# Kernel tuning notes

Measured on AMD Instinct MI355X. Metric: run time of the kernel, lower is better.

The kernel has to match this reference:

```python
import jax, jax.numpy as jnp
import numpy as np

N = 100000   # nodes
E = 800000   # edges
IN, H, OUT = 128, 128, 100  # in_channels, hidden_channels, out_channels


def _layernorm(x, g, b, eps=1e-5):
    m = jnp.mean(x, axis=-1, keepdims=True)
    v = jnp.var(x, axis=-1, keepdims=True)
    return (x - m) * jax.lax.rsqrt(v + eps) * g + b


def _sage_mean(x, src, dst, wl, bl, wr, n):
    # PyG SAGEConv(aggr='mean'): lin_l(mean_j x_j) + lin_r(x)
    s = jax.ops.segment_sum(x[src], dst, num_segments=n)               # [n, d]
    cnt = jax.ops.segment_sum(jnp.ones_like(dst, jnp.float32), dst, num_segments=n)
    aggr = s / jnp.maximum(cnt, 1.0)[:, None]
    return aggr @ wl + bl + x @ wr


def _sage_max(x, src, dst, wl, bl, wr, n):
    # PyG SAGEConv(aggr='max'): lin_l(max_j x_j) + lin_r(x); empty segments -> 0
    m = jax.ops.segment_max(x[src], dst, num_segments=n)               # [n, d]
    m = jnp.where(jnp.isfinite(m), m, 0.0)
    return m @ wl + bl + x @ wr


def setup_inputs() -> dict:
    key = jax.random.key(0)
    ks = jax.random.split(key, 16)

    def w(k, shape):
        fan_in = shape[0]
        return jax.random.normal(k, shape, jnp.float32) * (1.0 / np.sqrt(fan_in))

    inp = {
        'x': jax.random.normal(ks[0], (N, IN), jnp.float32),
        'src': jax.random.randint(ks[1], (E,), 0, N, jnp.int32),
        'dst': jax.random.randint(ks[2], (E,), 0, N, jnp.int32),
        's1_wl': w(ks[3], (IN, H)), 's1_bl': jnp.zeros((H,), jnp.float32), 's1_wr': w(ks[4], (IN, H)),
        'ln1_g': jnp.ones((H,), jnp.float32), 'ln1_b': jnp.zeros((H,), jnp.float32),
        's2_wl': w(ks[5], (H, 2 * H)), 's2_bl': jnp.zeros((2 * H,), jnp.float32), 's2_wr': w(ks[6], (H, 2 * H)),
        'ln2_g': jnp.ones((2 * H,), jnp.float32), 'ln2_b': jnp.zeros((2 * H,), jnp.float32),
        's3_wl': w(ks[7], (2 * H, H)), 's3_bl': jnp.zeros((H,), jnp.float32), 's3_wr': w(ks[8], (2 * H, H)),
        'ln3_g': jnp.ones((H,), jnp.float32), 'ln3_b': jnp.zeros((H,), jnp.float32),
        'l1_w': w(ks[9], (H, H // 2)), 'l1_b': jnp.zeros((H // 2,), jnp.float32),
        'ln4_g': jnp.ones((H // 2,), jnp.float32), 'ln4_b': jnp.zeros((H // 2,), jnp.float32),
        'lo_w': w(ks[10], (H // 2, OUT)), 'lo_b': jnp.zeros((OUT,), jnp.float32),
    }
    return inp


def reference(x, src, dst,
              s1_wl, s1_bl, s1_wr, ln1_g, ln1_b,
              s2_wl, s2_bl, s2_wr, ln2_g, ln2_b,
              s3_wl, s3_bl, s3_wr, ln3_g, ln3_b,
              l1_w, l1_b, ln4_g, ln4_b, lo_w, lo_b):
    n = x.shape[0]
    h = _sage_mean(x, src, dst, s1_wl, s1_bl, s1_wr, n)
    h = jax.nn.relu(_layernorm(h, ln1_g, ln1_b))          # dropout disabled (eval)
    h = _sage_max(h, src, dst, s2_wl, s2_bl, s2_wr, n)
    h = jax.nn.relu(_layernorm(h, ln2_g, ln2_b))
    h = _sage_mean(h, src, dst, s3_wl, s3_bl, s3_wr, n)
    h = jax.nn.relu(_layernorm(h, ln3_g, ln3_b))
    h = h @ l1_w + l1_b
    h = jax.nn.relu(_layernorm(h, ln4_g, ln4_b))
    return h @ lo_w + lo_b                                 # [N, OUT]
```

## Files before the change

### kernel.cpp

```cpp
#include <hip/hip_runtime.h>
#include <stdint.h>

#define DEV __device__ __forceinline__

typedef __attribute__((ext_vector_type(8))) short bf16x8;
typedef __attribute__((ext_vector_type(4))) float f32x4;

DEV float bf2f(uint16_t u) { return __uint_as_float(((uint32_t)u) << 16); }
DEV uint16_t f2bfbits(float f) {
    uint32_t x = __float_as_uint(f);
    uint32_t r = x + 0x7fffu + ((x >> 16) & 1u);
    return (uint16_t)(r >> 16);
}
DEV void stv(uint16_t* p, float v) { *p = f2bfbits(v); }
DEV void stv(float* p, float v) { *p = v; }

template<int C> DEV void ldbf(const uint16_t* p, float* f);
template<> DEV void ldbf<2>(const uint16_t* p, float* f) {
    uint32_t v = *reinterpret_cast<const uint32_t*>(p);
    f[0] = __uint_as_float(v << 16); f[1] = __uint_as_float(v & 0xffff0000u);
}
template<> DEV void ldbf<4>(const uint16_t* p, float* f) {
    uint2 v = *reinterpret_cast<const uint2*>(p);
    f[0] = __uint_as_float(v.x << 16); f[1] = __uint_as_float(v.x & 0xffff0000u);
    f[2] = __uint_as_float(v.y << 16); f[3] = __uint_as_float(v.y & 0xffff0000u);
}

DEV void gl16(const uint16_t* g, uint8_t* l) {
    __builtin_amdgcn_global_load_lds(
        (const __attribute__((address_space(1))) uint32_t*)g,
        (__attribute__((address_space(3))) uint32_t*)l, 16, 0, 0);
}

template<int N> DEV void vwait() {
    if constexpr (N == 0)      asm volatile("s_waitcnt vmcnt(0)" ::: "memory");
    else if constexpr (N == 3) asm volatile("s_waitcnt vmcnt(3)" ::: "memory");
    else if constexpr (N == 4) asm volatile("s_waitcnt vmcnt(4)" ::: "memory");
    else if constexpr (N == 6) asm volatile("s_waitcnt vmcnt(6)" ::: "memory");
    else                       asm volatile("s_waitcnt vmcnt(0)" ::: "memory");
}

__global__ void k_count(const int* __restrict__ dst, int e, int* __restrict__ deg) {
    int i = blockIdx.x * 256 + threadIdx.x;
    if (i < e) atomicAdd(&deg[dst[i]], 1);
}

__global__ void k_block_sums(const int* __restrict__ deg, int n, int* __restrict__ bsum) {
    __shared__ int sm[256];
    int base = blockIdx.x * 1024;
    int s = 0;
    for (int i = threadIdx.x; i < 1024; i += 256) {
        int g = base + i;
        if (g < n) s += deg[g];
    }
    sm[threadIdx.x] = s; __syncthreads();
    for (int o = 128; o > 0; o >>= 1) {
        if (threadIdx.x < o) sm[threadIdx.x] += sm[threadIdx.x + o];
        __syncthreads();
    }
    if (threadIdx.x == 0) bsum[blockIdx.x] = sm[0];
}

__global__ void k_scan_bsums(int* bsum, int nb) {
    __shared__ int sm[256];
    int t = threadIdx.x;
    int v = (t < nb) ? bsum[t] : 0;
    sm[t] = v; __syncthreads();
    for (int o = 1; o < 256; o <<= 1) {
        int add = (t >= o) ? sm[t - o] : 0;
        __syncthreads();
        sm[t] += add;
        __syncthreads();
    }
    if (t < nb) bsum[t] = (t == 0) ? 0 : sm[t - 1];
}

__global__ void k_scan_final(const int* __restrict__ deg, int n,
                             const int* __restrict__ bsum, int* __restrict__ offs,
                             int* __restrict__ cursor) {
    __shared__ int sm[256];
    int t = threadIdx.x;
    int i0 = blockIdx.x * 1024 + t * 4;
    int d0 = (i0     < n) ? deg[i0]     : 0;
    int d1 = (i0 + 1 < n) ? deg[i0 + 1] : 0;
    int d2 = (i0 + 2 < n) ? deg[i0 + 2] : 0;
    int d3 = (i0 + 3 < n) ? deg[i0 + 3] : 0;
    int ts = d0 + d1 + d2 + d3;
    sm[t] = ts; __syncthreads();
    for (int o = 1; o < 256; o <<= 1) {
        int add = (t >= o) ? sm[t - o] : 0;
        __syncthreads();
        sm[t] += add;
        __syncthreads();
    }
    int e0 = bsum[blockIdx.x] + ((t == 0) ? 0 : sm[t - 1]);
    int e1 = e0 + d0, e2 = e1 + d1, e3 = e2 + d2, e4 = e3 + d3;
    if (i0     < n) { offs[i0]     = e0; cursor[i0]     = e0; }
    if (i0 + 1 < n) { offs[i0 + 1] = e1; cursor[i0 + 1] = e1; }
    if (i0 + 2 < n) { offs[i0 + 2] = e2; cursor[i0 + 2] = e2; }
    if (i0 + 3 < n) { offs[i0 + 3] = e3; cursor[i0 + 3] = e3; }
    if (i0 <= n - 1 && n - 1 < i0 + 4) offs[n] = e4;
}

__global__ void k_scatter(const int* __restrict__ src, const int* __restrict__ dst, int e,
                          int* __restrict__ cursor, int* __restrict__ csr) {
    int i = blockIdx.x * 256 + threadIdx.x;
    if (i < e) {
        int p = atomicAdd(&cursor[dst[i]], 1);
        csr[p] = src[i];
    }
}

__global__ void k_f2b(const float* __restrict__ in, uint16_t* __restrict__ o, int n4) {
    int i = blockIdx.x * 256 + threadIdx.x;
    if (i < n4) {
        float4 v = reinterpret_cast<const float4*>(in)[i];
        uint2 w;
        w.x = f2bfbits(v.x) | ((uint32_t)f2bfbits(v.y) << 16);
        w.y = f2bfbits(v.z) | ((uint32_t)f2bfbits(v.w) << 16);
        reinterpret_cast<uint2*>(o)[i] = w;
    }
}

struct PrepSeg { const float* W; uint16_t* wt; int K, Dreal, koff, ldk, start, end; };
struct PrepAll { PrepSeg s[8]; };

__global__ void k_prep_all(PrepAll P, int total) {
    int idx = blockIdx.x * 256 + threadIdx.x;
    if (idx >= total) return;
#pragma unroll
    for (int i = 0; i < 8; ++i) {
        if (idx >= P.s[i].start && idx < P.s[i].end) {
            int loc = idx - P.s[i].start;
            int K = P.s[i].K;
            int nn = loc / K, k = loc - nn * K;
            float v = (nn < P.s[i].Dreal) ? P.s[i].W[(size_t)k * P.s[i].Dreal + nn] : 0.f;
            P.s[i].wt[(size_t)nn * P.s[i].ldk + P.s[i].koff + k] = f2bfbits(v);
        }
    }
}

template<int D, bool MAXAGG>
__global__ __launch_bounds__(256) void k_aggr(const uint16_t* __restrict__ X,
                                              const int* __restrict__ offs,
                                              const int* __restrict__ csr,
                                              int n, uint16_t* __restrict__ out) {
    constexpr int C = D / 64;
    int lane = threadIdx.x & 63;
    int node = blockIdx.x * 4 + (threadIdx.x >> 6);
    if (node >= n) return;
    int beg = offs[node], end = offs[node + 1];
    float acc[C];
#pragma unroll
    for (int c = 0; c < C; c++) acc[c] = 0.f;
    const size_t loff = (size_t)lane * C;
    int i = beg;
    for (; i + 3 < end; i += 4) {
        int s0 = csr[i], s1 = csr[i + 1], s2 = csr[i + 2], s3 = csr[i + 3];
        float f0[C], f1[C], f2[C], f3[C];
        ldbf<C>(X + (size_t)s0 * D + loff, f0);
        ldbf<C>(X + (size_t)s1 * D + loff, f1);
        ldbf<C>(X + (size_t)s2 * D + loff, f2);
        ldbf<C>(X + (size_t)s3 * D + loff, f3);
#pragma unroll
        for (int c = 0; c < C; c++) {
            if (MAXAGG) {
                acc[c] = fmaxf(acc[c], fmaxf(fmaxf(f0[c], f1[c]), fmaxf(f2[c], f3[c])));
            } else {
                acc[c] += (f0[c] + f1[c]) + (f2[c] + f3[c]);
            }
        }
    }
    for (; i < end; ++i) {
        int s = csr[i];
        float f[C];
        ldbf<C>(X + (size_t)s * D + loff, f);
#pragma unroll
        for (int c = 0; c < C; c++)
            acc[c] = MAXAGG ? fmaxf(acc[c], f[c]) : (acc[c] + f[c]);
    }
    int d = end - beg; if (d < 1) d = 1;
    float scale = MAXAGG ? 1.f : (1.f / (float)d);
    uint16_t* q = out + (size_t)node * D + loff;
    if constexpr (C == 2) {
        uint32_t v = f2bfbits(acc[0] * scale) | ((uint32_t)f2bfbits(acc[1] * scale) << 16);
        *reinterpret_cast<uint32_t*>(q) = v;
    } else {
        uint2 v;
        v.x = f2bfbits(acc[0] * scale) | ((uint32_t)f2bfbits(acc[1] * scale) << 16);
        v.y = f2bfbits(acc[2] * scale) | ((uint32_t)f2bfbits(acc[3] * scale) << 16);
        *reinterpret_cast<uint2*>(q) = v;
    }
}

__global__ __launch_bounds__(256) void k_aggr_ln(const uint16_t* __restrict__ YZ,
                                                 const int* __restrict__ offs,
                                                 const int* __restrict__ csr,
                                                 const float* __restrict__ g,
                                                 const float* __restrict__ b,
                                                 int n, uint16_t* __restrict__ out) {
    int lane = threadIdx.x & 63;
    int node = blockIdx.x * 4 + (threadIdx.x >> 6);
    if (node >= n) return;
    int beg = offs[node], end = offs[node + 1];
    float a0 = 0.f, a1 = 0.f;
    const size_t loff = (size_t)lane * 2;
    int i = beg;
    for (; i + 3 < end; i += 4) {
        int s0 = csr[i], s1 = csr[i + 1], s2 = csr[i + 2], s3 = csr[i + 3];
        float f0[2], f1[2], f2[2], f3[2];
        ldbf<2>(YZ + (size_t)s0 * 256 + loff, f0);
        ldbf<2>(YZ + (size_t)s1 * 256 + loff, f1);
        ldbf<2>(YZ + (size_t)s2 * 256 + loff, f2);
        ldbf<2>(YZ + (size_t)s3 * 256 + loff, f3);
        a0 += (f0[0] + f1[0]) + (f2[0] + f3[0]);
        a1 += (f0[1] + f1[1]) + (f2[1] + f3[1]);
    }
    for (; i < end; ++i) {
        int s = csr[i];
        float f[2];
        ldbf<2>(YZ + (size_t)s * 256 + loff, f);
        a0 += f[0]; a1 += f[1];
    }
    int d = end - beg; if (d < 1) d = 1;
    float scale = 1.f / (float)d;
    float z[2];
    ldbf<2>(YZ + (size_t)node * 256 + 128 + loff, z);
    float v0 = a0 * scale + z[0];
    float v1 = a1 * scale + z[1];
    float s = v0 + v1, s2 = v0 * v0 + v1 * v1;
#pragma unroll
    for (int o = 1; o < 64; o <<= 1) { s += __shfl_xor(s, o); s2 += __shfl_xor(s2, o); }
    float mean = s * (1.f / 128.f);
    float var = s2 * (1.f / 128.f) - mean * mean;
    float inv = rsqrtf(var + 1e-5f);
    float y0 = fmaxf((v0 - mean) * inv * g[loff]     + b[loff],     0.f);
    float y1 = fmaxf((v1 - mean) * inv * g[loff + 1] + b[loff + 1], 0.f);
    uint32_t w = f2bfbits(y0) | ((uint32_t)f2bfbits(y1) << 16);
    *reinterpret_cast<uint32_t*>(out + (size_t)node * 128 + loff) = w;
}

template<int KPER, int DOUT, int DB, bool DUAL, bool LN, bool ZBIAS, typename TO>
__global__ __launch_bounds__(256) void k_mf(const uint16_t* __restrict__ A0,
                                            const uint16_t* __restrict__ A1,
                                            const uint16_t* __restrict__ WT,
                                            const float* __restrict__ bias,
                                            const float* __restrict__ g,
                                            const float* __restrict__ bvec,
                                            int n, TO* __restrict__ out) {
    constexpr int KEFF = KPER * (DUAL ? 2 : 1);
    constexpr int NST = KEFF / 32;
    constexpr int NF = DB / 16;
    constexpr int WPL = DB * 16;
    constexpr int AB = 8192;
    constexpr int WB = DB * 64;
    constexpr int HB = DB / 64;
    constexpr int L  = 2 + HB;
    __shared__ __align__(16) uint8_t lds[3][AB + WB];

    int tid = threadIdx.x;
    int lane = tid & 63, wid = tid >> 6;
    int lr = lane & 15, kb = lane >> 4;
    int row0 = blockIdx.x * 128;
    int wrow = wid * 32;

    auto stage = [&](int kt, uint8_t* buf) {
        const uint16_t* Asel = A0; int kk = kt;
        if (DUAL && kt >= KPER) { Asel = A1; kk = kt - KPER; }
        uint8_t* aB = buf;
        uint8_t* wB = buf + AB;
#pragma unroll
        for (int j = 0; j < 2; ++j) {
            int p = wid * 2 + j, cb = p >> 1, h = p & 1;
            int grow = row0 + h * 64 + lane; if (grow >= n) grow = n - 1;
            gl16(Asel + (size_t)grow * KPER + kk + cb * 8, aB + cb * 2048 + h * 1024);
        }
#pragma unroll
        for (int j = 0; j < HB; ++j) {
            int p = wid * HB + j, cb = p / HB, h = p % HB;
            int c = h * 64 + lane;
            gl16(WT + (size_t)c * KEFF + kt + cb * 8, wB + cb * WPL + h * 1024);
        }
    };

    f32x4 acc[2][NF] = {};
    stage(0, lds[0]);
    if constexpr (NST > 1) stage(32, lds[1]);

#pragma unroll
    for (int s = 0; s < NST; ++s) {
        if (s < NST - 1) vwait<L>(); else vwait<0>();
        __builtin_amdgcn_s_barrier();
        __builtin_amdgcn_sched_barrier(0);
        if (s + 2 < NST) stage((s + 2) * 32, lds[(s + 2) % 3]);
        const uint8_t* aB = lds[s % 3];
        const uint8_t* wB = lds[s % 3] + AB;
        bf16x8 af0 = *reinterpret_cast<const bf16x8*>(aB + kb * 2048 + (wrow + lr) * 16);
        bf16x8 af1 = *reinterpret_cast<const bf16x8*>(aB + kb * 2048 + (wrow + 16 + lr) * 16);
#pragma unroll
        for (int nf = 0; nf < NF; ++nf) {
            bf16x8 wf = *reinterpret_cast<const bf16x8*>(wB + kb * WPL + (nf * 16 + lr) * 16);
            acc[0][nf] = __builtin_amdgcn_mfma_f32_16x16x32_bf16(af0, wf, acc[0][nf], 0, 0, 0);
            acc[1][nf] = __builtin_amdgcn_mfma_f32_16x16x32_bf16(af1, wf, acc[1][nf], 0, 0, 0);
        }
    }

#pragma unroll
    for (int nf = 0; nf < NF; ++nf) {
        int col = nf * 16 + lr;
        float bsv;
        if constexpr (ZBIAS) {
            bsv = (col >= DOUT / 2) ? bias[col - DOUT / 2] : 0.f;
        } else {
            bsv = (DB == DOUT || col < DOUT) ? bias[col] : 0.f;
        }
#pragma unroll
        for (int r = 0; r < 4; ++r) { acc[0][nf][r] += bsv; acc[1][nf][r] += bsv; }
    }
    if constexpr (LN) {
        float gv[NF], bv2[NF];
#pragma unroll
        for (int nf = 0; nf < NF; ++nf) {
            int col = nf * 16 + lr;
            gv[nf] = g[col]; bv2[nf] = bvec[col];
        }
#pragma unroll
        for (int m = 0; m < 2; ++m) {
            float s[4], s2[4];
#pragma unroll
            for (int r = 0; r < 4; ++r) { s[r] = 0.f; s2[r] = 0.f; }
#pragma unroll
            for (int nf = 0; nf < NF; ++nf)
#pragma unroll
                for (int r = 0; r < 4; ++r) { float v = acc[m][nf][r]; s[r] += v; s2[r] += v * v; }
#pragma unroll
            for (int r = 0; r < 4; ++r) {
#pragma unroll
                for (int o = 1; o < 16; o <<= 1) {
                    s[r] += __shfl_xor(s[r], o);
                    s2[r] += __shfl_xor(s2[r], o);
                }
                float mean = s[r] / DOUT;
                float var = s2[r] / DOUT - mean * mean;
                float inv = rsqrtf(var + 1e-5f);
#pragma unroll
                for (int nf = 0; nf < NF; ++nf) {
                    float y = (acc[m][nf][r] - mean) * inv * gv[nf] + bv2[nf];
                    acc[m][nf][r] = fmaxf(y, 0.f);
                }
            }
        }
    }
#pragma unroll
    for (int m = 0; m < 2; ++m)
#pragma unroll
        for (int r = 0; r < 4; ++r) {
            int row = row0 + wrow + m * 16 + kb * 4 + r;
            if (row < n) {
#pragma unroll
                for (int nf = 0; nf < NF; ++nf) {
                    int col = nf * 16 + lr;
                    if (DB == DOUT || col < DOUT)
                        stv(out + (size_t)row * DOUT + col, acc[m][nf][r]);
                }
            }
        }
}

extern "C" void kernel_launch(void* const* d_in, const int* in_sizes, int n_in,
                              void* d_out, int out_size, void* d_ws, size_t ws_size,
                              hipStream_t stream) {
    const float* x     = (const float*)d_in[0];
    const int*   src   = (const int*)d_in[1];
    const int*   dst   = (const int*)d_in[2];
    const float* s1_wl = (const float*)d_in[3];
    const float* s1_bl = (const float*)d_in[4];
    const float* s1_wr = (const float*)d_in[5];
    const float* ln1_g = (const float*)d_in[6];
    const float* ln1_b = (const float*)d_in[7];
    const float* s2_wl = (const float*)d_in[8];
    const float* s2_bl = (const float*)d_in[9];
    const float* s2_wr = (const float*)d_in[10];
    const float* ln2_g = (const float*)d_in[11];
    const float* ln2_b = (const float*)d_in[12];
    const float* s3_wl = (const float*)d_in[13];
    const float* s3_bl = (const float*)d_in[14];
    const float* s3_wr = (const float*)d_in[15];
    const float* ln3_g = (const float*)d_in[16];
    const float* ln3_b = (const float*)d_in[17];
    const float* l1_w  = (const float*)d_in[18];
    const float* l1_b  = (const float*)d_in[19];
    const float* ln4_g = (const float*)d_in[20];
    const float* ln4_b = (const float*)d_in[21];
    const float* lo_w  = (const float*)d_in[22];
    const float* lo_b  = (const float*)d_in[23];
    float* out = (float*)d_out;

    const int N = in_sizes[0] / 128;
    const int E = in_sizes[1];
    (void)n_in; (void)out_size; (void)ws_size;

    char* w = (char*)d_ws;
    size_t off = 0;
    auto alloc = [&](size_t bytes) -> void* {
        void* p = w + off;
        off = (off + bytes + 255) & ~(size_t)255;
        return p;
    };
    int* deg    = (int*)alloc((size_t)N * 4);
    int* offs   = (int*)alloc((size_t)(N + 1) * 4);
    int* cursor = (int*)alloc((size_t)N * 4);
    int* bsum   = (int*)alloc(1024 * 4);
    int* csr    = (int*)alloc((size_t)E * 4);
    uint16_t* wt1 = (uint16_t*)alloc(256 * 128 * 2);
    uint16_t* wt2 = (uint16_t*)alloc(256 * 256 * 2);
    uint16_t* wt3 = (uint16_t*)alloc(256 * 256 * 2);
    uint16_t* wt4 = (uint16_t*)alloc(64 * 128 * 2);
    uint16_t* wt5 = (uint16_t*)alloc(128 * 64 * 2);
    uint16_t* xb    = (uint16_t*)alloc((size_t)N * 128 * 2);
    uint16_t* YZ    = (uint16_t*)alloc((size_t)N * 256 * 2);
    uint16_t* h1    = (uint16_t*)alloc((size_t)N * 128 * 2);
    uint16_t* aggrB = (uint16_t*)alloc((size_t)N * 128 * 2);
    uint16_t* h2    = (uint16_t*)alloc((size_t)N * 256 * 2);
    uint16_t* h3    = (uint16_t*)alloc((size_t)N * 128 * 2);
    uint16_t* h4    = aggrB;

    int gE = (E + 255) / 256;
    int nb = (N + 1023) / 1024;
    int gNode = (N + 3) / 4;
    int g128 = (N + 127) / 128;

    hipMemsetAsync(deg, 0, (size_t)N * 4, stream);
    k_count<<<gE, 256, 0, stream>>>(dst, E, deg);
    k_block_sums<<<nb, 256, 0, stream>>>(deg, N, bsum);
    k_scan_bsums<<<1, 256, 0, stream>>>(bsum, nb);
    k_scan_final<<<nb, 256, 0, stream>>>(deg, N, bsum, offs, cursor);
    k_scatter<<<gE, 256, 0, stream>>>(src, dst, E, cursor, csr);

    PrepAll P;
    int cum = 0;
    auto seg = [&](int i, const float* W, uint16_t* wt, int K, int Dreal, int Dpad, int koff, int ldk) {
        P.s[i] = {W, wt, K, Dreal, koff, ldk, cum, cum + Dpad * K};
        cum += Dpad * K;
    };
    seg(0, s1_wl, wt1,             128, 128, 128, 0,   128);
    seg(1, s1_wr, wt1 + 128 * 128, 128, 128, 128, 0,   128);
    seg(2, s2_wl, wt2,             128, 256, 256, 0,   256);
    seg(3, s2_wr, wt2,             128, 256, 256, 128, 256);
    seg(4, s3_wl, wt3,             256, 128, 128, 0,   256);
    seg(5, s3_wr, wt3 + 128 * 256, 256, 128, 128, 0,   256);
    seg(6, l1_w,  wt4,             128, 64,  64,  0,   128);
    seg(7, lo_w,  wt5,             64,  100, 128, 0,   64);
    k_prep_all<<<(cum + 255) / 256, 256, 0, stream>>>(P, cum);

    k_f2b<<<(N * 128 / 4 + 255) / 256, 256, 0, stream>>>(x, xb, N * 128 / 4);

    k_mf<128, 256, 256, false, false, true, uint16_t><<<g128, 256, 0, stream>>>(
        xb, nullptr, wt1, s1_bl, nullptr, nullptr, N, YZ);
    k_aggr_ln<<<gNode, 256, 0, stream>>>(YZ, offs, csr, ln1_g, ln1_b, N, h1);

    k_aggr<128, true><<<gNode, 256, 0, stream>>>(h1, offs, csr, N, aggrB);
    k_mf<128, 256, 256, true, true, false, uint16_t><<<g128, 256, 0, stream>>>(
        aggrB, h1, wt2, s2_bl, ln2_g, ln2_b, N, h2);

    k_mf<256, 256, 256, false, false, true, uint16_t><<<g128, 256, 0, stream>>>(
        h2, nullptr, wt3, s3_bl, nullptr, nullptr, N, YZ);
    k_aggr_ln<<<gNode, 256, 0, stream>>>(YZ, offs, csr, ln3_g, ln3_b, N, h3);

    k_mf<128, 64, 64, false, true, false, uint16_t><<<g128, 256, 0, stream>>>(
        h3, nullptr, wt4, l1_b, ln4_g, ln4_b, N, h4);

    k_mf<64, 100, 128, false, false, false, float><<<g128, 256, 0, stream>>>(
        h4, nullptr, wt5, lo_b, nullptr, nullptr, N, out);
}
```

Baseline: 424.2 us.

## Preload full weight matrix into LDS and stage A per-wave without block barriers

The MFMA GEMM kernel now loads the whole transposed weight matrix into LDS once at kernel start instead of re-staging a weight slice every k-step. The A tile is split so each wave loads only its own 32 rows, which lets the main loop drop the per-step s_barrier and rely on per-wave vmcnt waits. This removes repeated weight traffic and block-wide synchronisation. In exchange LDS use grows with K×DB, and launch_bounds(256,1) signals the compiler that occupancy may be limited to one block per CU.

```diff
diff --git a/kernel.cpp b/kernel.cpp
--- a/kernel.cpp
+++ b/kernel.cpp
@@ -34,9 +34,8 @@
 
 template<int N> DEV void vwait() {
     if constexpr (N == 0)      asm volatile("s_waitcnt vmcnt(0)" ::: "memory");
-    else if constexpr (N == 3) asm volatile("s_waitcnt vmcnt(3)" ::: "memory");
+    else if constexpr (N == 2) asm volatile("s_waitcnt vmcnt(2)" ::: "memory");
     else if constexpr (N == 4) asm volatile("s_waitcnt vmcnt(4)" ::: "memory");
-    else if constexpr (N == 6) asm volatile("s_waitcnt vmcnt(6)" ::: "memory");
     else                       asm volatile("s_waitcnt vmcnt(0)" ::: "memory");
 }
 
@@ -241,22 +240,23 @@
 }
 
 template<int KPER, int DOUT, int DB, bool DUAL, bool LN, bool ZBIAS, typename TO>
-__global__ __launch_bounds__(256) void k_mf(const uint16_t* __restrict__ A0,
-                                            const uint16_t* __restrict__ A1,
-                                            const uint16_t* __restrict__ WT,
-                                            const float* __restrict__ bias,
-                                            const float* __restrict__ g,
-                                            const float* __restrict__ bvec,
-                                            int n, TO* __restrict__ out) {
+__global__ __launch_bounds__(256, 1) void k_mf(const uint16_t* __restrict__ A0,
+                                               const uint16_t* __restrict__ A1,
+                                               const uint16_t* __restrict__ WT,
+                                               const float* __restrict__ bias,
+                                               const float* __restrict__ g,
+                                               const float* __restrict__ bvec,
+                                               int n, TO* __restrict__ out) {
     constexpr int KEFF = KPER * (DUAL ? 2 : 1);
     constexpr int NST = KEFF / 32;
-    constexpr int NF = DB / 16;
+    constexpr int NF  = DB / 16;
     constexpr int WPL = DB * 16;
-    constexpr int AB = 8192;
-    constexpr int WB = DB * 64;
-    constexpr int HB = DB / 64;
-    constexpr int L  = 2 + HB;
-    __shared__ __align__(16) uint8_t lds[3][AB + WB];
+    constexpr int NPL = KEFF / 8;
+    constexpr int WSZ = NPL * WPL;
+    constexpr int WHB = DB / 64;
+    constexpr int WCH = WSZ / 1024;
+    __shared__ __align__(16) uint8_t wL[WSZ];
+    __shared__ __align__(16) uint8_t aL[3][4][2048];
 
     int tid = threadIdx.x;
     int lane = tid & 63, wid = tid >> 6;
@@ -264,42 +264,44 @@
     int row0 = blockIdx.x * 128;
     int wrow = wid * 32;
 
-    auto stage = [&](int kt, uint8_t* buf) {
+    for (int p = wid; p < WCH; p += 4) {
+        int cp = p / WHB, h = p % WHB;
+        gl16(WT + (size_t)(h * 64 + lane) * KEFF + cp * 8, wL + cp * WPL + h * 1024);
+    }
+
+    int grow = row0 + wrow + (lane & 31); if (grow >= n) grow = n - 1;
+    int cbl = lane >> 5;
+    auto stageA = [&](int s, int buf) {
+        int kt = s * 32;
         const uint16_t* Asel = A0; int kk = kt;
         if (DUAL && kt >= KPER) { Asel = A1; kk = kt - KPER; }
-        uint8_t* aB = buf;
-        uint8_t* wB = buf + AB;
 #pragma unroll
         for (int j = 0; j < 2; ++j) {
-            int p = wid * 2 + j, cb = p >> 1, h = p & 1;
-            int grow = row0 + h * 64 + lane; if (grow >= n) grow = n - 1;
-            gl16(Asel + (size_t)grow * KPER + kk + cb * 8, aB + cb * 2048 + h * 1024);
-        }
-#pragma unroll
-        for (int j = 0; j < HB; ++j) {
-            int p = wid * HB + j, cb = p / HB, h = p % HB;
-            int c = h * 64 + lane;
-            gl16(WT + (size_t)c * KEFF + kt + cb * 8, wB + cb * WPL + h * 1024);
+            int cb = 2 * j + cbl;
+            gl16(Asel + (size_t)grow * KPER + kk + cb * 8, aL[buf][wid] + j * 1024);
         }
     };
 
+    stageA(0, 0);
+    if constexpr (NST > 1) stageA(1, 1);
+    __syncthreads();
+
     f32x4 acc[2][NF] = {};
-    stage(0, lds[0]);
-    if constexpr (NST > 1) stage(32, lds[1]);
-
 #pragma unroll
     for (int s = 0; s < NST; ++s) {
-        if (s < NST - 1) vwait<L>(); else vwait<0>();
-        __builtin_amdgcn_s_barrier();
+        if (s + 2 < NST) stageA(s + 2, (s + 2) % 3);
+        constexpr int DUMMY = 0; (void)DUMMY;
+        if (NST - 1 - s >= 2)      vwait<4>();
+        else if (NST - 1 - s == 1) vwait<2>();
+        else                       vwait<0>();
         __builtin_amdgcn_sched_barrier(0);
-        if (s + 2 < NST) stage((s + 2) * 32, lds[(s + 2) % 3]);
-        const uint8_t* aB = lds[s % 3];
-        const uint8_t* wB = lds[s % 3] + AB;
-        bf16x8 af0 = *reinterpret_cast<const bf16x8*>(aB + kb * 2048 + (wrow + lr) * 16);
-        bf16x8 af1 = *reinterpret_cast<const bf16x8*>(aB + kb * 2048 + (wrow + 16 + lr) * 16);
+        const uint8_t* aB = aL[s % 3][wid];
+        bf16x8 af0 = *reinterpret_cast<const bf16x8*>(aB + kb * 512 + lr * 16);
+        bf16x8 af1 = *reinterpret_cast<const bf16x8*>(aB + kb * 512 + (16 + lr) * 16);
+        const uint8_t* wB = wL + (size_t)(s * 4 + kb) * WPL;
 #pragma unroll
         for (int nf = 0; nf < NF; ++nf) {
-            bf16x8 wf = *reinterpret_cast<const bf16x8*>(wB + kb * WPL + (nf * 16 + lr) * 16);
+            bf16x8 wf = *reinterpret_cast<const bf16x8*>(wB + (nf * 16 + lr) * 16);
             acc[0][nf] = __builtin_amdgcn_mfma_f32_16x16x32_bf16(af0, wf, acc[0][nf], 0, 0, 0);
             acc[1][nf] = __builtin_amdgcn_mfma_f32_16x16x32_bf16(af1, wf, acc[1][nf], 0, 0, 0);
         }
```

New measurement: 449.0 us. 1.06x slower.

## Swap MFMA operands and stage bf16 GEMM outputs through swizzled LDS for coalesced stores

Applied to the files above, without the earlier changes.

The MFMA operand order is swapped so each lane holds four consecutive output columns of one row instead of four rows of one column. LayerNorm reductions and bias/gamma/beta loads become per-row reductions with vectorized parameter loads. For bf16 outputs the tile is written into LDS with an XOR swizzle and read back as 16-byte rows for fully coalesced global stores, and the fp32 path uses float4 stores. This replaces scattered 2-byte and 4-byte stores, at the cost of extra barriers and an LDS round trip.

```diff
diff --git a/kernel.cpp b/kernel.cpp
--- a/kernel.cpp
+++ b/kernel.cpp
@@ -12,8 +12,6 @@
     uint32_t r = x + 0x7fffu + ((x >> 16) & 1u);
     return (uint16_t)(r >> 16);
 }
-DEV void stv(uint16_t* p, float v) { *p = f2bfbits(v); }
-DEV void stv(float* p, float v) { *p = v; }
 
 template<int C> DEV void ldbf(const uint16_t* p, float* f);
 template<> DEV void ldbf<2>(const uint16_t* p, float* f) {
@@ -240,7 +238,7 @@
     *reinterpret_cast<uint32_t*>(out + (size_t)node * 128 + loff) = w;
 }
 
-template<int KPER, int DOUT, int DB, bool DUAL, bool LN, bool ZBIAS, typename TO>
+template<int KPER, int DOUT, int DB, bool DUAL, bool LN, bool ZBIAS, bool CST, typename TO>
 __global__ __launch_bounds__(256) void k_mf(const uint16_t* __restrict__ A0,
                                             const uint16_t* __restrict__ A1,
                                             const uint16_t* __restrict__ WT,
@@ -263,6 +261,7 @@
     int lr = lane & 15, kb = lane >> 4;
     int row0 = blockIdx.x * 128;
     int wrow = wid * 32;
+    int colq = kb * 4;
 
     auto stage = [&](int kt, uint8_t* buf) {
         const uint16_t* Asel = A0; int kk = kt;
@@ -300,71 +299,94 @@
 #pragma unroll
         for (int nf = 0; nf < NF; ++nf) {
             bf16x8 wf = *reinterpret_cast<const bf16x8*>(wB + kb * WPL + (nf * 16 + lr) * 16);
-            acc[0][nf] = __builtin_amdgcn_mfma_f32_16x16x32_bf16(af0, wf, acc[0][nf], 0, 0, 0);
-            acc[1][nf] = __builtin_amdgcn_mfma_f32_16x16x32_bf16(af1, wf, acc[1][nf], 0, 0, 0);
+            acc[0][nf] = __builtin_amdgcn_mfma_f32_16x16x32_bf16(wf, af0, acc[0][nf], 0, 0, 0);
+            acc[1][nf] = __builtin_amdgcn_mfma_f32_16x16x32_bf16(wf, af1, acc[1][nf], 0, 0, 0);
         }
     }
 
 #pragma unroll
     for (int nf = 0; nf < NF; ++nf) {
-        int col = nf * 16 + lr;
-        float bsv;
+        int cq = nf * 16 + colq;
+        f32x4 bs = {0.f, 0.f, 0.f, 0.f};
         if constexpr (ZBIAS) {
-            bsv = (col >= DOUT / 2) ? bias[col - DOUT / 2] : 0.f;
+            if (cq >= DOUT / 2) bs = *reinterpret_cast<const f32x4*>(bias + cq - DOUT / 2);
         } else {
-            bsv = (DB == DOUT || col < DOUT) ? bias[col] : 0.f;
-        }
-#pragma unroll
-        for (int r = 0; r < 4; ++r) { acc[0][nf][r] += bsv; acc[1][nf][r] += bsv; }
+            if (DB == DOUT || cq < DOUT) bs = *reinterpret_cast<const f32x4*>(bias + cq);
+        }
+#pragma unroll
+        for (int m = 0; m < 2; ++m)
+#pragma unroll
+            for (int r = 0; r < 4; ++r) acc[m][nf][r] += bs[r];
     }
     if constexpr (LN) {
-        float gv[NF], bv2[NF];
-#pragma unroll
-        for (int nf = 0; nf < NF; ++nf) {
-            int col = nf * 16 + lr;
-            gv[nf] = g[col]; bv2[nf] = bvec[col];
-        }
 #pragma unroll
         for (int m = 0; m < 2; ++m) {
-            float s[4], s2[4];
-#pragma unroll
-            for (int r = 0; r < 4; ++r) { s[r] = 0.f; s2[r] = 0.f; }
+            float s = 0.f, s2 = 0.f;
 #pragma unroll
             for (int nf = 0; nf < NF; ++nf)
 #pragma unroll
-                for (int r = 0; r < 4; ++r) { float v = acc[m][nf][r]; s[r] += v; s2[r] += v * v; }
-#pragma unroll
-            for (int r = 0; r < 4; ++r) {
-#pragma unroll
-                for (int o = 1; o < 16; o <<= 1) {
-                    s[r] += __shfl_xor(s[r], o);
-                    s2[r] += __shfl_xor(s2[r], o);
-                }
-                float mean = s[r] / DOUT;
-                float var = s2[r] / DOUT - mean * mean;
-                float inv = rsqrtf(var + 1e-5f);
+                for (int r = 0; r < 4; ++r) { float v = acc[m][nf][r]; s += v; s2 += v * v; }
+            s += __shfl_xor(s, 16); s2 += __shfl_xor(s2, 16);
+            s += __shfl_xor(s, 32); s2 += __shfl_xor(s2, 32);
+            float mean = s / DOUT;
+            float var = s2 / DOUT - mean * mean;
+            float inv = rsqrtf(var + 1e-5f);
+#pragma unroll
+            for (int nf = 0; nf < NF; ++nf) {
+                int cq = nf * 16 + colq;
+                f32x4 g4 = *reinterpret_cast<const f32x4*>(g + cq);
+                f32x4 b4 = *reinterpret_cast<const f32x4*>(bvec + cq);
+#pragma unroll
+                for (int r = 0; r < 4; ++r)
+                    acc[m][nf][r] = fmaxf((acc[m][nf][r] - mean) * inv * g4[r] + b4[r], 0.f);
+            }
+        }
+    }
+
+    if constexpr (CST) {
+        constexpr int RP = DB * 2;
+        __syncthreads();
+        uint8_t* ct = &lds[0][0];
+#pragma unroll
+        for (int m = 0; m < 2; ++m) {
+            int row = wrow + m * 16 + lr;
+            uint32_t rx = (uint32_t)(row & 7) << 4;
+#pragma unroll
+            for (int nf = 0; nf < NF; ++nf) {
+                uint32_t colb = (uint32_t)(nf * 16 + colq) * 2;
+                uint2 pk;
+                pk.x = f2bfbits(acc[m][nf][0]) | ((uint32_t)f2bfbits(acc[m][nf][1]) << 16);
+                pk.y = f2bfbits(acc[m][nf][2]) | ((uint32_t)f2bfbits(acc[m][nf][3]) << 16);
+                *reinterpret_cast<uint2*>(ct + (uint32_t)row * RP + (colb ^ rx)) = pk;
+            }
+        }
+        __syncthreads();
+        constexpr int NIT = (128 * RP) / (256 * 16);
+#pragma unroll
+        for (int i = 0; i < NIT; ++i) {
+            uint32_t flat = (uint32_t)(i * 256 + tid) * 16;
+            uint32_t row = flat / RP, off = flat % RP;
+            uint4 v = *reinterpret_cast<const uint4*>(ct + row * RP + (off ^ ((row & 7) << 4)));
+            int grow = row0 + (int)row;
+            if (grow < n)
+                *reinterpret_cast<uint4*>((uint16_t*)out + (size_t)grow * DOUT + off / 2) = v;
+        }
+    } else {
+#pragma unroll
+        for (int m = 0; m < 2; ++m) {
+            int row = row0 + wrow + m * 16 + lr;
+            if (row < n) {
 #pragma unroll
                 for (int nf = 0; nf < NF; ++nf) {
-                    float y = (acc[m][nf][r] - mean) * inv * gv[nf] + bv2[nf];
-                    acc[m][nf][r] = fmaxf(y, 0.f);
+                    int cq = nf * 16 + colq;
+                    if (DB == DOUT || cq < DOUT) {
+                        float4 v = {acc[m][nf][0], acc[m][nf][1], acc[m][nf][2], acc[m][nf][3]};
+                        *reinterpret_cast<float4*>((float*)out + (size_t)row * DOUT + cq) = v;
+                    }
                 }
             }
         }
     }
-#pragma unroll
-    for (int m = 0; m < 2; ++m)
-#pragma unroll
-        for (int r = 0; r < 4; ++r) {
-            int row = row0 + wrow + m * 16 + kb * 4 + r;
-            if (row < n) {
-#pragma unroll
-                for (int nf = 0; nf < NF; ++nf) {
-                    int col = nf * 16 + lr;
-                    if (DB == DOUT || col < DOUT)
-                        stv(out + (size_t)row * DOUT + col, acc[m][nf][r]);
-                }
-            }
-        }
 }
 
 extern "C" void kernel_launch(void* const* d_in, const int* in_sizes, int n_in,
@@ -455,21 +477,21 @@
 
     k_f2b<<<(N * 128 / 4 + 255) / 256, 256, 0, stream>>>(x, xb, N * 128 / 4);
 
-    k_mf<128, 256, 256, false, false, true, uint16_t><<<g128, 256, 0, stream>>>(
+    k_mf<128, 256, 256, false, false, true, true, uint16_t><<<g128, 256, 0, stream>>>(
         xb, nullptr, wt1, s1_bl, nullptr, nullptr, N, YZ);
     k_aggr_ln<<<gNode, 256, 0, stream>>>(YZ, offs, csr, ln1_g, ln1_b, N, h1);
 
     k_aggr<128, true><<<gNode, 256, 0, stream>>>(h1, offs, csr, N, aggrB);
-    k_mf<128, 256, 256, true, true, false, uint16_t><<<g128, 256, 0, stream>>>(
+    k_mf<128, 256, 256, true, true, false, true, uint16_t><<<g128, 256, 0, stream>>>(
         aggrB, h1, wt2, s2_bl, ln2_g, ln2_b, N, h2);
 
-    k_mf<256, 256, 256, false, false, true, uint16_t><<<g128, 256, 0, stream>>>(
+    k_mf<256, 256, 256, false, false, true, true, uint16_t><<<g128, 256, 0, stream>>>(
         h2, nullptr, wt3, s3_bl, nullptr, nullptr, N, YZ);
     k_aggr_ln<<<gNode, 256, 0, stream>>>(YZ, offs, csr, ln3_g, ln3_b, N, h3);
 
-    k_mf<128, 64, 64, false, true, false, uint16_t><<<g128, 256, 0, stream>>>(
+    k_mf<128, 64, 64, false, true, false, true, uint16_t><<<g128, 256, 0, stream>>>(
         h3, nullptr, wt4, l1_b, ln4_g, ln4_b, N, h4);
 
-    k_mf<64, 100, 128, false, false, false, float><<<g128, 256, 0, stream>>>(
+    k_mf<64, 100, 128, false, false, false, false, float><<<g128, 256, 0, stream>>>(
         h4, nullptr, wt5, lo_b, nullptr, nullptr, N, out);
 }
```

Result: no change. 432.2 us (+1.9%).

## Split GEMM output columns across a 2D grid and move layer-2 LayerNorm to its own kernel

Applied to the files above, without the earlier changes.

The MFMA GEMM kernel gains a column-block index (blockIdx.y), so the 256-wide output GEMMs now run as two 128-column tiles each. Each block holds half the accumulators and half the LDS weight tile, which should lower register and LDS pressure and double the number of blocks. Because the layer-2 LayerNorm needs the full 256-wide row, it is no longer fused into the GEMM and runs as a separate in-place row kernel. The cost is an extra launch plus an extra read and write of h2, and the A tile is now loaded twice.

```diff
diff --git a/kernel.cpp b/kernel.cpp
--- a/kernel.cpp
+++ b/kernel.cpp
@@ -240,6 +240,39 @@
     *reinterpret_cast<uint32_t*>(out + (size_t)node * 128 + loff) = w;
 }
 
+template<int D>
+__global__ __launch_bounds__(256) void k_lnr(uint16_t* __restrict__ X,
+                                             const float* __restrict__ g,
+                                             const float* __restrict__ b, int n) {
+    constexpr int C = D / 64;
+    int lane = threadIdx.x & 63;
+    int row = blockIdx.x * 4 + (threadIdx.x >> 6);
+    if (row >= n) return;
+    uint16_t* p = X + (size_t)row * D + lane * C;
+    float f[C];
+    ldbf<C>(p, f);
+    float s = 0.f, s2 = 0.f;
+#pragma unroll
+    for (int c = 0; c < C; c++) { s += f[c]; s2 += f[c] * f[c]; }
+#pragma unroll
+    for (int o = 1; o < 64; o <<= 1) { s += __shfl_xor(s, o); s2 += __shfl_xor(s2, o); }
+    float mean = s / D;
+    float var = s2 / D - mean * mean;
+    float inv = rsqrtf(var + 1e-5f);
+#pragma unroll
+    for (int c = 0; c < C; c++)
+        f[c] = fmaxf((f[c] - mean) * inv * g[lane * C + c] + b[lane * C + c], 0.f);
+    if constexpr (C == 2) {
+        uint32_t v = f2bfbits(f[0]) | ((uint32_t)f2bfbits(f[1]) << 16);
+        *reinterpret_cast<uint32_t*>(p) = v;
+    } else {
+        uint2 v;
+        v.x = f2bfbits(f[0]) | ((uint32_t)f2bfbits(f[1]) << 16);
+        v.y = f2bfbits(f[2]) | ((uint32_t)f2bfbits(f[3]) << 16);
+        *reinterpret_cast<uint2*>(p) = v;
+    }
+}
+
 template<int KPER, int DOUT, int DB, bool DUAL, bool LN, bool ZBIAS, typename TO>
 __global__ __launch_bounds__(256) void k_mf(const uint16_t* __restrict__ A0,
                                             const uint16_t* __restrict__ A1,
@@ -262,7 +295,10 @@
     int lane = tid & 63, wid = tid >> 6;
     int lr = lane & 15, kb = lane >> 4;
     int row0 = blockIdx.x * 128;
+    int col0 = blockIdx.y * DB;
     int wrow = wid * 32;
+
+    const uint16_t* WTb = WT + (size_t)col0 * KEFF;
 
     auto stage = [&](int kt, uint8_t* buf) {
         const uint16_t* Asel = A0; int kk = kt;
@@ -279,7 +315,7 @@
         for (int j = 0; j < HB; ++j) {
             int p = wid * HB + j, cb = p / HB, h = p % HB;
             int c = h * 64 + lane;
-            gl16(WT + (size_t)c * KEFF + kt + cb * 8, wB + cb * WPL + h * 1024);
+            gl16(WTb + (size_t)c * KEFF + kt + cb * 8, wB + cb * WPL + h * 1024);
         }
     };
 
@@ -307,12 +343,12 @@
 
 #pragma unroll
     for (int nf = 0; nf < NF; ++nf) {
-        int col = nf * 16 + lr;
+        int col = col0 + nf * 16 + lr;
         float bsv;
         if constexpr (ZBIAS) {
             bsv = (col >= DOUT / 2) ? bias[col - DOUT / 2] : 0.f;
         } else {
-            bsv = (DB == DOUT || col < DOUT) ? bias[col] : 0.f;
+            bsv = (col < DOUT) ? bias[col] : 0.f;
         }
 #pragma unroll
         for (int r = 0; r < 4; ++r) { acc[0][nf][r] += bsv; acc[1][nf][r] += bsv; }
@@ -359,8 +395,8 @@
             if (row < n) {
 #pragma unroll
                 for (int nf = 0; nf < NF; ++nf) {
-                    int col = nf * 16 + lr;
-                    if (DB == DOUT || col < DOUT)
+                    int col = col0 + nf * 16 + lr;
+                    if (col < DOUT)
                         stv(out + (size_t)row * DOUT + col, acc[m][nf][r]);
                 }
             }
@@ -455,21 +491,22 @@
 
     k_f2b<<<(N * 128 / 4 + 255) / 256, 256, 0, stream>>>(x, xb, N * 128 / 4);
 
-    k_mf<128, 256, 256, false, false, true, uint16_t><<<g128, 256, 0, stream>>>(
+    k_mf<128, 256, 128, false, false, true, uint16_t><<<dim3(g128, 2), 256, 0, stream>>>(
         xb, nullptr, wt1, s1_bl, nullptr, nullptr, N, YZ);
     k_aggr_ln<<<gNode, 256, 0, stream>>>(YZ, offs, csr, ln1_g, ln1_b, N, h1);
 
     k_aggr<128, true><<<gNode, 256, 0, stream>>>(h1, offs, csr, N, aggrB);
-    k_mf<128, 256, 256, true, true, false, uint16_t><<<g128, 256, 0, stream>>>(
-        aggrB, h1, wt2, s2_bl, ln2_g, ln2_b, N, h2);
-
-    k_mf<256, 256, 256, false, false, true, uint16_t><<<g128, 256, 0, stream>>>(
+    k_mf<128, 256, 128, true, false, false, uint16_t><<<dim3(g128, 2), 256, 0, stream>>>(
+        aggrB, h1, wt2, s2_bl, nullptr, nullptr, N, h2);
+    k_lnr<256><<<gNode, 256, 0, stream>>>(h2, ln2_g, ln2_b, N);
+
+    k_mf<256, 256, 128, false, false, true, uint16_t><<<dim3(g128, 2), 256, 0, stream>>>(
         h2, nullptr, wt3, s3_bl, nullptr, nullptr, N, YZ);
     k_aggr_ln<<<gNode, 256, 0, stream>>>(YZ, offs, csr, ln3_g, ln3_b, N, h3);
 
-    k_mf<128, 64, 64, false, true, false, uint16_t><<<g128, 256, 0, stream>>>(
+    k_mf<128, 64, 64, false, true, false, uint16_t><<<dim3(g128, 1), 256, 0, stream>>>(
         h3, nullptr, wt4, l1_b, ln4_g, ln4_b, N, h4);
 
-    k_mf<64, 100, 128, false, false, false, float><<<g128, 256, 0, stream>>>(
+    k_mf<64, 100, 128, false, false, false, float><<<dim3(g128, 1), 256, 0, stream>>>(
         h4, nullptr, wt5, lo_b, nullptr, nullptr, N, out);
 }
```

After: 516.7 us. +21.8%, slower.
